# Kernel optimization log

Hardware: AMD Instinct MI355X
Metric: run time of the kernel (lower is better)

Reference implementation:

```python
import jax, jax.numpy as jnp
import numpy as np
from math import sqrt

B, N, CS, H, D, K = 8, 256, 512, 8, 64, 32
NB = 2 * K + 1          # no_bins = 65
CT = 2048               # c_transition
INF = 1e9
WL = sqrt(0.5)          # w_L
EPS = 1e-5


def setup_inputs() -> dict:
    key = jax.random.key(0)
    ks = jax.random.split(key, 10)
    sc = 0.02
    return {
        "s": jax.random.normal(ks[0], (B, N, CS), jnp.float32),
        "masks": jnp.ones((B, N), jnp.bool_),
        "wq": jax.random.normal(ks[1], (CS, D * H), jnp.float32) * sc,
        "wk": jax.random.normal(ks[2], (CS, D * H), jnp.float32) * sc,
        "wv": jax.random.normal(ks[3], (CS, D * H), jnp.float32) * sc,
        "wb": jax.random.normal(ks[4], (NB, H), jnp.float32) * sc,
        "wo": jax.random.normal(ks[5], ((NB + D) * H, CS), jnp.float32) * sc,
        "bo": jnp.zeros((CS,), jnp.float32),
        "ln1_g": jnp.ones((CS,), jnp.float32),
        "ln1_b": jnp.zeros((CS,), jnp.float32),
        "w1": jax.random.normal(ks[6], (CS, CT), jnp.float32) * sc,
        "b1": jnp.zeros((CT,), jnp.float32),
        "w2": jax.random.normal(ks[7], (CT, CS), jnp.float32) * sc,
        "b2": jnp.zeros((CS,), jnp.float32),
        "ln2_g": jnp.ones((CS,), jnp.float32),
        "ln2_b": jnp.zeros((CS,), jnp.float32),
    }


def _layernorm(x, g, b):
    m = jnp.mean(x, -1, keepdims=True)
    v = jnp.var(x, -1, keepdims=True)
    return (x - m) * jax.lax.rsqrt(v + EPS) * g + b


def _heads(x):  # [B,N,D*H] -> [B,H,N,D]  (torch: reshape(B,N,D,H) then move H forward)
    return jnp.transpose(x.reshape(B, N, D, H), (0, 3, 1, 2))


def reference(s, masks, wq, wk, wv, wb, wo, bo, ln1_g, ln1_b, w1, b1, w2, b2, ln2_g, ln2_b):
    mf = masks.astype(s.dtype)                       # [B,N]
    sq = mf[:, :, None] * mf[:, None, :]             # [B,N,N]

    # relative position one-hot, clipped to [-K, K] -> [N,N,NB]
    r = jnp.arange(N)
    dmat = jnp.clip(r[:, None] - r[None, :], -K, K) + K
    relpos_base = jax.nn.one_hot(dmat, NB, dtype=s.dtype)
    relpos = relpos_base[None] * sq[..., None]       # [B,N,N,NB]

    b_bias = jnp.einsum('bijc,ch->bhij', relpos, wb)  # [B,H,N,N]

    q = _heads(s @ wq)                               # [B,H,N,D]
    k = _heads(s @ wk)
    v = _heads(s @ wv)

    logits = WL * (jnp.einsum('bhid,bhjd->bhij', q, k) / sqrt(D) + b_bias)
    logits = logits - INF * (1.0 - sq)[:, None]      # mask
    a = jax.nn.softmax(logits, axis=-1)              # [B,H,N,N]

    # pairwise aggregation and value aggregation (einsum avoids [B,H,N,N,NB] blowup)
    o_pair = jnp.einsum('bhij,bijc->bhic', a, relpos)  # [B,H,N,NB]
    o = jnp.einsum('bhij,bhjd->bhid', a, v)            # [B,H,N,D]

    op = jnp.transpose(o_pair, (0, 2, 1, 3)).reshape(B, N, H * NB)
    ov = jnp.transpose(o, (0, 2, 1, 3)).reshape(B, N, H * D)
    embd = jnp.concatenate([op, ov], axis=-1) @ wo + bo   # [B,N,CS]

    x = _layernorm(s + embd, ln1_g, ln1_b)
    ff = jax.nn.relu(x @ w1 + b1) @ w2 + b2
    x = _layernorm(x + ff, ln2_g, ln2_b)
    return x, a
```

## Files before the change

### kernel.cpp

```cpp
#include <hip/hip_runtime.h>
#include <hip/hip_bf16.h>
#include <cstdint>

#define B_ 8
#define N_ 256
#define CS_ 512
#define H_ 8
#define D_ 64
#define K_ 32
#define NB_ 65
#define CT_ 2048
#define WL_ 0.70710678118654752f

typedef __attribute__((ext_vector_type(8))) short bf16x8;
typedef __attribute__((ext_vector_type(4))) float f32x4;

#define GLOBAL_AS __attribute__((address_space(1)))
#define LDS_AS __attribute__((address_space(3)))

__device__ __forceinline__ void async16(void* lds, const void* g) {
  __builtin_amdgcn_global_load_lds((const GLOBAL_AS uint32_t*)g,
                                   (LDS_AS uint32_t*)lds, 16, 0, 0);
}

__device__ __forceinline__ ushort f2bf(float v) {
  __hip_bfloat16 hb = __float2bfloat16(v);
  return *(ushort*)&hb;
}

__global__ __launch_bounds__(128) void gemm_bf16(
    const ushort* __restrict__ A, const ushort* __restrict__ Bt,
    const float* __restrict__ bias, float* __restrict__ C,
    ushort* __restrict__ Cb, int M, int Nc, int Kd, int flags) {
  __shared__ ushort As[64 * 64];
  __shared__ ushort Bs[128 * 64];
  int tid = threadIdx.x;
  int bm = blockIdx.y * 64, bn = blockIdx.x * 128;
  int S = gridDim.z, z = blockIdx.z;
  int T = Kd >> 6;
  int it0 = (z * T) / S, it1 = ((z + 1) * T) / S;
  if (flags & 8) C += (size_t)z * M * Nc;
  int w = tid >> 6, l = tid & 63;
  int lm = l & 15, lq = l >> 4;
  int srow = tid >> 3;
  int sg = tid & 7;

  f32x4 acc[4][4];
#pragma unroll
  for (int i = 0; i < 4; ++i)
#pragma unroll
    for (int j = 0; j < 4; ++j) acc[i][j] = (f32x4){0.f, 0.f, 0.f, 0.f};

  for (int it = it0; it < it1; ++it) {
    int k0 = it << 6;
    __syncthreads();
#pragma unroll
    for (int r = 0; r < 4; ++r) {
      int row = r * 16 + srow;
      int gl = sg ^ (row & 7);
      async16(&As[row * 64 + sg * 8],
              A + (size_t)(bm + row) * Kd + k0 + gl * 8);
    }
#pragma unroll
    for (int r = 0; r < 8; ++r) {
      int row = r * 16 + srow;
      int gl = sg ^ (row & 7);
      async16(&Bs[row * 64 + sg * 8],
              Bt + (size_t)(bn + row) * Kd + k0 + gl * 8);
    }
    __syncthreads();
#pragma unroll
    for (int kk = 0; kk < 2; ++kk) {
      bf16x8 af[4], bfr[4];
#pragma unroll
      for (int i = 0; i < 4; ++i) {
        int ma = 16 * i + lm;
        af[i] = *(const bf16x8*)&As[ma * 64 + ((kk * 4 + lq) ^ (ma & 7)) * 8];
        int nb = w * 64 + 16 * i + lm;
        bfr[i] = *(const bf16x8*)&Bs[nb * 64 + ((kk * 4 + lq) ^ (nb & 7)) * 8];
      }
#pragma unroll
      for (int i = 0; i < 4; ++i)
#pragma unroll
        for (int j = 0; j < 4; ++j)
          acc[i][j] = __builtin_amdgcn_mfma_f32_16x16x32_bf16(
              af[i], bfr[j], acc[i][j], 0, 0, 0);
    }
  }
#pragma unroll
  for (int j = 0; j < 4; ++j) {
    int col = bn + w * 64 + 16 * j + lm;
    float bv = ((flags & 1) && z == 0) ? bias[col] : 0.f;
#pragma unroll
    for (int i = 0; i < 4; ++i) {
#pragma unroll
      for (int r = 0; r < 4; ++r) {
        int row = bm + 16 * i + lq * 4 + r;
        float v = acc[i][j][r] + bv;
        if (flags & 2) v = fmaxf(v, 0.f);
        if (flags & 8) C[(size_t)row * Nc + col] = v;
        if (flags & 4) Cb[(size_t)row * Nc + col] = f2bf(v);
        if (flags & 16) {
          int which = col >> 9, c = col & 511;
          int hh = c >> 6, d2 = c & 63;
          int bb = row >> 8, nn = row & 255;
          size_t dst;
          if (which == 2)
            dst = (size_t)2 * 1048576 + (((size_t)(bb * 8 + hh) * 64) + d2) * 256 + nn;
          else
            dst = (size_t)which * 1048576 + (((size_t)(bb * 8 + hh) * 256) + nn) * 64 + d2;
          Cb[dst] = f2bf(v);
        }
      }
    }
  }
}

__global__ __launch_bounds__(256) void prep_all(
    const float* __restrict__ s, __hip_bfloat16* __restrict__ s_bf,
    const float* __restrict__ wq, const float* __restrict__ wk,
    const float* __restrict__ wv, const float* __restrict__ wo,
    const float* __restrict__ w1, const float* __restrict__ w2,
    __hip_bfloat16* __restrict__ wqkvT, __hip_bfloat16* __restrict__ wopT,
    __hip_bfloat16* __restrict__ w1T, __hip_bfloat16* __restrict__ w2T) {
  int blk = blockIdx.x;
  if (blk < 1024) {
    int i = blk * 256 + threadIdx.x;
    float4 v = ((const float4*)s)[i];
    s_bf[i * 4 + 0] = __float2bfloat16(v.x);
    s_bf[i * 4 + 1] = __float2bfloat16(v.y);
    s_bf[i * 4 + 2] = __float2bfloat16(v.z);
    s_bf[i * 4 + 3] = __float2bfloat16(v.w);
    return;
  }
  blk -= 1024;
  __shared__ float tile[32][33];
  const float* src;
  __hip_bfloat16* dst;
  int R, C, Kpad, tX, tIdx, whichBase = -1;
  if (blk < 768) {
    int zz = blk >> 8; tIdx = blk & 255;
    src = zz == 0 ? wq : zz == 1 ? wk : wv;
    dst = wqkvT; whichBase = zz * 512; R = 512; C = 512; Kpad = 512; tX = 16;
  } else if (blk < 1312) {
    tIdx = blk - 768; src = wo; dst = wopT; R = 1032; C = 512; Kpad = 1088; tX = 16;
  } else if (blk < 2336) {
    tIdx = blk - 1312; src = w1; dst = w1T; R = 512; C = 2048; Kpad = 512; tX = 64;
  } else {
    tIdx = blk - 2336; src = w2; dst = w2T; R = 2048; C = 512; Kpad = 2048; tX = 16;
  }
  int c0 = (tIdx % tX) * 32, r0 = (tIdx / tX) * 32;
  int tx = threadIdx.x & 31, ty = threadIdx.x >> 5;
#pragma unroll
  for (int yy = 0; yy < 32; yy += 8) {
    int r = r0 + ty + yy, c = c0 + tx;
    tile[ty + yy][tx] = (r < R && c < C) ? src[(size_t)r * C + c] : 0.f;
  }
  __syncthreads();
#pragma unroll
  for (int yy = 0; yy < 32; yy += 8) {
    int cc = c0 + ty + yy, k = r0 + tx;
    if (cc < C && k < Kpad) {
      int n = (whichBase >= 0) ? (whichBase + (cc & 7) * 64 + (cc >> 3)) : cc;
      dst[(size_t)n * Kpad + k] = __float2bfloat16(tile[tx][ty + yy]);
    }
  }
}

__global__ __launch_bounds__(256) void attn_fused(
    const ushort* __restrict__ qh, const ushort* __restrict__ kh,
    const ushort* __restrict__ vT, const int* __restrict__ masks,
    const float* __restrict__ wb, float* __restrict__ a_out,
    ushort* __restrict__ cat) {
  int strip = blockIdx.x & 3, bh = blockIdx.x >> 2;
  int h = bh & 7, b = bh >> 3;
  __shared__ ushort Ks[256 * 64];
  __shared__ ushort Ps[64 * 64];
  __shared__ float wbs[NB_];
  __shared__ float mfj[256];
  int tid = threadIdx.x;
  int srow = tid >> 3, sg = tid & 7;
#pragma unroll
  for (int rr = 0; rr < 8; ++rr) {
    int row = rr * 32 + srow;
    int gl = sg ^ (row & 7);
    async16(&Ks[row * 64 + sg * 8],
            kh + ((size_t)bh * 256 + row) * 64 + gl * 8);
  }
  int w = tid >> 6, l = tid & 63, lm = l & 15, lq = l >> 4;
  bf16x8 qf[2];
  {
    const ushort* qrow =
        qh + ((size_t)bh * 256 + strip * 64 + w * 16 + lm) * 64 + lq * 8;
    qf[0] = *(const bf16x8*)qrow;
    qf[1] = *(const bf16x8*)(qrow + 32);
  }
  if (tid < NB_) wbs[tid] = wb[tid * H_ + h];
  mfj[tid] = (masks[b * 256 + tid] != 0) ? 1.f : 0.f;
  __syncthreads();

  f32x4 acc[16];
#pragma unroll
  for (int ct = 0; ct < 16; ++ct) {
    int krow = ct * 16 + lm;
    bf16x8 kf0 = *(const bf16x8*)&Ks[krow * 64 + ((lq) ^ (krow & 7)) * 8];
    bf16x8 kf1 = *(const bf16x8*)&Ks[krow * 64 + ((4 + lq) ^ (krow & 7)) * 8];
    f32x4 zf = (f32x4){0.f, 0.f, 0.f, 0.f};
    zf = __builtin_amdgcn_mfma_f32_16x16x32_bf16(qf[0], kf0, zf, 0, 0, 0);
    acc[ct] = __builtin_amdgcn_mfma_f32_16x16x32_bf16(qf[1], kf1, zf, 0, 0, 0);
  }
  int ibase = strip * 64 + w * 16 + lq * 4;
  float mfi[4];
#pragma unroll
  for (int r = 0; r < 4; ++r) mfi[r] = mfj[ibase + r];
#pragma unroll
  for (int ct = 0; ct < 16; ++ct) {
    int j = ct * 16 + lm;
    float mj = mfj[j];
#pragma unroll
    for (int r = 0; r < 4; ++r) {
      int i = ibase + r;
      int diff = i - j;
      int cb = diff < -K_ ? 0 : (diff > K_ ? 2 * K_ : diff + K_);
      float sq = mfi[r] * mj;
      acc[ct][r] = WL_ * (acc[ct][r] * 0.125f + wbs[cb] * sq) - 1e9f * (1.f - sq);
    }
  }
  float mx[4], sm[4];
#pragma unroll
  for (int r = 0; r < 4; ++r) {
    float m = acc[0][r];
#pragma unroll
    for (int ct = 1; ct < 16; ++ct) m = fmaxf(m, acc[ct][r]);
#pragma unroll
    for (int o = 1; o < 16; o <<= 1) m = fmaxf(m, __shfl_xor(m, o, 64));
    mx[r] = m;
  }
#pragma unroll
  for (int ct = 0; ct < 16; ++ct)
#pragma unroll
    for (int r = 0; r < 4; ++r) acc[ct][r] = __expf(acc[ct][r] - mx[r]);
#pragma unroll
  for (int r = 0; r < 4; ++r) {
    float s = 0.f;
#pragma unroll
    for (int ct = 0; ct < 16; ++ct) s += acc[ct][r];
#pragma unroll
    for (int o = 1; o < 16; o <<= 1) s += __shfl_xor(s, o, 64);
    sm[r] = 1.f / s;
  }
  float p0[4] = {0.f, 0.f, 0.f, 0.f}, p64[4] = {0.f, 0.f, 0.f, 0.f};
#pragma unroll
  for (int ct = 0; ct < 16; ++ct) {
    int j = ct * 16 + lm;
    float mj = mfj[j];
#pragma unroll
    for (int r = 0; r < 4; ++r) {
      int i = ibase + r;
      float aval = acc[ct][r] * sm[r];
      a_out[((size_t)bh * 256 + i) * 256 + j] = aval;
      float val = aval * mfi[r] * mj;
      int diff = i - j;
      if (diff <= -K_)      p0[r] += val;
      else if (diff >= K_)  p64[r] += val;
      else cat[((size_t)(b * 256 + i)) * 1088 + h * 65 + diff + K_] = f2bf(val);
    }
  }
#pragma unroll
  for (int r = 0; r < 4; ++r)
#pragma unroll
    for (int o = 1; o < 16; o <<= 1) {
      p0[r]  += __shfl_xor(p0[r], o, 64);
      p64[r] += __shfl_xor(p64[r], o, 64);
    }
  if (lm == 0) {
#pragma unroll
    for (int r = 0; r < 4; ++r) {
      int i = ibase + r;
      cat[((size_t)(b * 256 + i)) * 1088 + h * 65 + 0]      = f2bf(p0[r]);
      cat[((size_t)(b * 256 + i)) * 1088 + h * 65 + 2 * K_] = f2bf(p64[r]);
    }
  }
#pragma unroll
  for (int r = 0; r < 4; ++r) {
    int i = ibase + r;
#pragma unroll
    for (int t = 0; t < 4; ++t) {
      int c = 1 + lm + 16 * t;
      if (c < 64) {
        int j = i - c + K_;
        if (j < 0 || j > 255)
          cat[((size_t)(b * 256 + i)) * 1088 + h * 65 + c] = 0;
      }
    }
  }
  if (h == 0) {
    for (int idx = tid; idx < 64 * 56; idx += 256) {
      int r = idx / 56, c = 1032 + (idx - r * 56);
      cat[((size_t)(b * 256 + strip * 64 + r)) * 1088 + c] = 0;
    }
  }
  f32x4 acc2[4];
#pragma unroll
  for (int nt = 0; nt < 4; ++nt) acc2[nt] = (f32x4){0.f, 0.f, 0.f, 0.f};
  const ushort* vbase = vT + (size_t)bh * 16384;
#pragma unroll
  for (int qt = 0; qt < 4; ++qt) {
    bf16x8 vf0[4], vf1[4];
#pragma unroll
    for (int nt = 0; nt < 4; ++nt) {
      const ushort* vrow = vbase + (size_t)(nt * 16 + lm) * 256 + qt * 64 + lq * 8;
      vf0[nt] = *(const bf16x8*)vrow;
      vf1[nt] = *(const bf16x8*)(vrow + 32);
    }
#pragma unroll
    for (int ctl = 0; ctl < 4; ++ctl) {
      int ct = qt * 4 + ctl;
#pragma unroll
      for (int r = 0; r < 4; ++r) {
        int rowl = w * 16 + lq * 4 + r;
        int g = ctl * 2 + (lm >> 3);
        Ps[rowl * 64 + ((g ^ (rowl & 7)) << 3) + (lm & 7)] =
            f2bf(acc[ct][r] * sm[r]);
      }
    }
    int prow = w * 16 + lm;
#pragma unroll
    for (int kst = 0; kst < 2; ++kst) {
      bf16x8 af = *(const bf16x8*)&Ps[prow * 64 + (((kst * 4 + lq) ^ (prow & 7)) << 3)];
#pragma unroll
      for (int nt = 0; nt < 4; ++nt)
        acc2[nt] = __builtin_amdgcn_mfma_f32_16x16x32_bf16(
            af, kst ? vf1[nt] : vf0[nt], acc2[nt], 0, 0, 0);
    }
  }
#pragma unroll
  for (int nt = 0; nt < 4; ++nt) {
    int d = nt * 16 + lm;
#pragma unroll
    for (int r = 0; r < 4; ++r) {
      int i = ibase + r;
      cat[((size_t)(b * 256 + i)) * 1088 + 520 + h * 64 + d] = f2bf(acc2[nt][r]);
    }
  }
}

__device__ __forceinline__ float lnReduceSum(float v, float* red) {
#pragma unroll
  for (int o = 32; o > 0; o >>= 1) v += __shfl_xor(v, o, 64);
  int w = threadIdx.x >> 6;
  __syncthreads();
  if ((threadIdx.x & 63) == 0) red[w] = v;
  __syncthreads();
  return red[0] + red[1] + red[2] + red[3];
}

__global__ __launch_bounds__(256) void ln_sum(
    const float* __restrict__ x1, const float* __restrict__ xp,
    int S, int stride, const float* __restrict__ g,
    const float* __restrict__ bta, float* __restrict__ out,
    __hip_bfloat16* __restrict__ out_bf) {
  __shared__ float red[4];
  int row = blockIdx.x, tid = threadIdx.x;
  size_t base = (size_t)row * 512;
  float v0 = x1[base + tid];
  float v1 = x1[base + tid + 256];
  for (int s = 0; s < S; ++s) {
    v0 += xp[(size_t)s * stride + base + tid];
    v1 += xp[(size_t)s * stride + base + tid + 256];
  }
  float su = lnReduceSum(v0 + v1, red);
  float sq = lnReduceSum(v0 * v0 + v1 * v1, red);
  float mean = su * (1.f / 512.f);
  float var = sq * (1.f / 512.f) - mean * mean;
  float inv = rsqrtf(var + 1e-5f);
  float o0 = (v0 - mean) * inv * g[tid] + bta[tid];
  float o1 = (v1 - mean) * inv * g[tid + 256] + bta[tid + 256];
  out[base + tid]       = o0;
  out[base + tid + 256] = o1;
  if (out_bf) {
    out_bf[base + tid]       = __float2bfloat16(o0);
    out_bf[base + tid + 256] = __float2bfloat16(o1);
  }
}

extern "C" void kernel_launch(void* const* d_in, const int* in_sizes, int n_in,
                              void* d_out, int out_size, void* d_ws, size_t ws_size,
                              hipStream_t stream) {
  const float* s     = (const float*)d_in[0];
  const int*   masks = (const int*)d_in[1];
  const float* wq = (const float*)d_in[2];
  const float* wk = (const float*)d_in[3];
  const float* wv = (const float*)d_in[4];
  const float* wb = (const float*)d_in[5];
  const float* wo = (const float*)d_in[6];
  const float* bo = (const float*)d_in[7];
  const float* ln1_g = (const float*)d_in[8];
  const float* ln1_b = (const float*)d_in[9];
  const float* w1 = (const float*)d_in[10];
  const float* b1 = (const float*)d_in[11];
  const float* w2 = (const float*)d_in[12];
  const float* b2 = (const float*)d_in[13];
  const float* ln2_g = (const float*)d_in[14];
  const float* ln2_b = (const float*)d_in[15];

  float* out_x = (float*)d_out;
  float* out_a = out_x + 1048576;

  float* ws = (float*)d_ws;
  float* embd_part = ws + 0;
  float* xbuf      = ws + 4194304;
  float* ff_part   = ws + 5242880;
  ushort* qkv_bf   = (ushort*)(ws + 9437184);
  ushort* q_bf = qkv_bf;
  ushort* k_bf = qkv_bf + 1048576;
  ushort* v_bf = qkv_bf + 2097152;
  ushort* cat_bf = (ushort*)(ws + 10223616);
  __hip_bfloat16* h_bf  = (__hip_bfloat16*)(ws + 11337728);
  __hip_bfloat16* s_bf  = (__hip_bfloat16*)(ws + 13434880);
  __hip_bfloat16* x_bf  = (__hip_bfloat16*)(ws + 13959168);
  __hip_bfloat16* wqkvT = (__hip_bfloat16*)(ws + 14483456);
  __hip_bfloat16* wopT  = (__hip_bfloat16*)(ws + 14876672);
  __hip_bfloat16* w1T   = (__hip_bfloat16*)(ws + 15155200);
  __hip_bfloat16* w2T   = (__hip_bfloat16*)(ws + 15679488);

  dim3 blk(256), blkg(128);
  prep_all<<<dim3(4384), blk, 0, stream>>>(s, s_bf, wq, wk, wv, wo, w1, w2,
                                           wqkvT, wopT, w1T, w2T);
  gemm_bf16<<<dim3(12, 32, 1), blkg, 0, stream>>>(
      (const ushort*)s_bf, (const ushort*)wqkvT, nullptr, nullptr,
      qkv_bf, 2048, 1536, 512, 16);
  attn_fused<<<dim3(256), blk, 0, stream>>>(q_bf, k_bf, v_bf, masks, wb,
                                            out_a, cat_bf);
  gemm_bf16<<<dim3(4, 32, 4), blkg, 0, stream>>>(
      cat_bf, (const ushort*)wopT, bo, embd_part, nullptr,
      2048, 512, 1088, 1 | 8);
  ln_sum<<<dim3(2048), blk, 0, stream>>>(s, embd_part, 4, 1048576,
                                         ln1_g, ln1_b, xbuf, x_bf);
  gemm_bf16<<<dim3(16, 32, 1), blkg, 0, stream>>>(
      (const ushort*)x_bf, (const ushort*)w1T, b1, nullptr, (ushort*)h_bf,
      2048, 2048, 512, 1 | 2 | 4);
  gemm_bf16<<<dim3(4, 32, 4), blkg, 0, stream>>>(
      (const ushort*)h_bf, (const ushort*)w2T, b2, ff_part, nullptr,
      2048, 512, 2048, 1 | 8);
  ln_sum<<<dim3(2048), blk, 0, stream>>>(xbuf, ff_part, 4, 1048576,
                                         ln2_g, ln2_b, out_x, nullptr);
}
```

Baseline: 194.7 us.

## Stage GEMM bf16 epilogues through LDS, vectorize LN/prep, halve attention block rows

```diff
diff --git a/kernel.cpp b/kernel.cpp
--- a/kernel.cpp
+++ b/kernel.cpp
@@ -87,32 +87,82 @@
               af[i], bfr[j], acc[i][j], 0, 0, 0);
     }
   }
+
+  int bcol0 = bn + w * 64;
+  int lr = l >> 3, lc = l & 7;
+  ushort* Tb = &Bs[w * 4096];
+
+  if (flags & 16) {
+    int which = bcol0 >> 9;
+    int hh = (bcol0 & 511) >> 6;
+    int b = bm >> 8, nn0 = bm & 255;
+    if (which == 2) {
+#pragma unroll
+      for (int j = 0; j < 4; ++j)
+#pragma unroll
+        for (int i = 0; i < 4; ++i) {
+          ushort pk[4];
+#pragma unroll
+          for (int r = 0; r < 4; ++r) pk[r] = f2bf(acc[i][j][r]);
+          *(uint2*)&Tb[(16 * j + lm) * 64 + 16 * i + lq * 4] = *(uint2*)pk;
+        }
+    } else {
+#pragma unroll
+      for (int j = 0; j < 4; ++j)
+#pragma unroll
+        for (int i = 0; i < 4; ++i)
+#pragma unroll
+          for (int r = 0; r < 4; ++r)
+            Tb[(16 * i + lq * 4 + r) * 64 + 16 * j + lm] = f2bf(acc[i][j][r]);
+    }
+    __asm__ __volatile__("" ::: "memory");
+    ushort* dstb = Cb + (size_t)which * 1048576 + (size_t)(b * 8 + hh) * 16384;
+#pragma unroll
+    for (int p = 0; p < 8; ++p) {
+      int rowL = p * 8 + lr;
+      bf16x8 vv = *(const bf16x8*)&Tb[rowL * 64 + lc * 8];
+      if (which == 2)
+        *(bf16x8*)(dstb + (size_t)rowL * 256 + nn0 + lc * 8) = vv;
+      else
+        *(bf16x8*)(dstb + (size_t)(nn0 + rowL) * 64 + lc * 8) = vv;
+    }
+    return;
+  }
+  if (flags & 4) {
+#pragma unroll
+    for (int j = 0; j < 4; ++j) {
+      float bv = ((flags & 1) && z == 0) ? bias[bcol0 + 16 * j + lm] : 0.f;
+#pragma unroll
+      for (int i = 0; i < 4; ++i)
+#pragma unroll
+        for (int r = 0; r < 4; ++r) {
+          float v = acc[i][j][r] + bv;
+          if (flags & 2) v = fmaxf(v, 0.f);
+          Tb[(16 * i + lq * 4 + r) * 64 + 16 * j + lm] = f2bf(v);
+        }
+    }
+    __asm__ __volatile__("" ::: "memory");
+#pragma unroll
+    for (int p = 0; p < 8; ++p) {
+      int rowL = p * 8 + lr;
+      bf16x8 vv = *(const bf16x8*)&Tb[rowL * 64 + lc * 8];
+      *(bf16x8*)(Cb + (size_t)(bm + rowL) * Nc + bcol0 + lc * 8) = vv;
+    }
+    return;
+  }
 #pragma unroll
   for (int j = 0; j < 4; ++j) {
-    int col = bn + w * 64 + 16 * j + lm;
+    int col = bcol0 + 16 * j + lm;
     float bv = ((flags & 1) && z == 0) ? bias[col] : 0.f;
 #pragma unroll
-    for (int i = 0; i < 4; ++i) {
+    for (int i = 0; i < 4; ++i)
 #pragma unroll
       for (int r = 0; r < 4; ++r) {
         int row = bm + 16 * i + lq * 4 + r;
         float v = acc[i][j][r] + bv;
         if (flags & 2) v = fmaxf(v, 0.f);
-        if (flags & 8) C[(size_t)row * Nc + col] = v;
-        if (flags & 4) Cb[(size_t)row * Nc + col] = f2bf(v);
-        if (flags & 16) {
-          int which = col >> 9, c = col & 511;
-          int hh = c >> 6, d2 = c & 63;
-          int bb = row >> 8, nn = row & 255;
-          size_t dst;
-          if (which == 2)
-            dst = (size_t)2 * 1048576 + (((size_t)(bb * 8 + hh) * 64) + d2) * 256 + nn;
-          else
-            dst = (size_t)which * 1048576 + (((size_t)(bb * 8 + hh) * 256) + nn) * 64 + d2;
-          Cb[dst] = f2bf(v);
-        }
+        C[(size_t)row * Nc + col] = v;
       }
-    }
   }
 }
 
@@ -124,16 +174,16 @@
     __hip_bfloat16* __restrict__ wqkvT, __hip_bfloat16* __restrict__ wopT,
     __hip_bfloat16* __restrict__ w1T, __hip_bfloat16* __restrict__ w2T) {
   int blk = blockIdx.x;
-  if (blk < 1024) {
+  if (blk < 512) {
     int i = blk * 256 + threadIdx.x;
-    float4 v = ((const float4*)s)[i];
-    s_bf[i * 4 + 0] = __float2bfloat16(v.x);
-    s_bf[i * 4 + 1] = __float2bfloat16(v.y);
-    s_bf[i * 4 + 2] = __float2bfloat16(v.z);
-    s_bf[i * 4 + 3] = __float2bfloat16(v.w);
+    float4 a = ((const float4*)s)[i * 2];
+    float4 c = ((const float4*)s)[i * 2 + 1];
+    ushort pk[8] = {f2bf(a.x), f2bf(a.y), f2bf(a.z), f2bf(a.w),
+                    f2bf(c.x), f2bf(c.y), f2bf(c.z), f2bf(c.w)};
+    *(uint4*)&((ushort*)s_bf)[i * 8] = *(uint4*)pk;
     return;
   }
-  blk -= 1024;
+  blk -= 512;
   __shared__ float tile[32][33];
   const float* src;
   __hip_bfloat16* dst;
@@ -167,22 +217,22 @@
   }
 }
 
-__global__ __launch_bounds__(256) void attn_fused(
+__global__ __launch_bounds__(128) void attn_fused(
     const ushort* __restrict__ qh, const ushort* __restrict__ kh,
     const ushort* __restrict__ vT, const int* __restrict__ masks,
     const float* __restrict__ wb, float* __restrict__ a_out,
     ushort* __restrict__ cat) {
-  int strip = blockIdx.x & 3, bh = blockIdx.x >> 2;
+  int strip = blockIdx.x & 7, bh = blockIdx.x >> 3;
   int h = bh & 7, b = bh >> 3;
   __shared__ ushort Ks[256 * 64];
-  __shared__ ushort Ps[64 * 64];
+  __shared__ ushort Ps[32 * 64];
   __shared__ float wbs[NB_];
   __shared__ float mfj[256];
   int tid = threadIdx.x;
   int srow = tid >> 3, sg = tid & 7;
 #pragma unroll
-  for (int rr = 0; rr < 8; ++rr) {
-    int row = rr * 32 + srow;
+  for (int rr = 0; rr < 16; ++rr) {
+    int row = rr * 16 + srow;
     int gl = sg ^ (row & 7);
     async16(&Ks[row * 64 + sg * 8],
             kh + ((size_t)bh * 256 + row) * 64 + gl * 8);
@@ -191,12 +241,13 @@
   bf16x8 qf[2];
   {
     const ushort* qrow =
-        qh + ((size_t)bh * 256 + strip * 64 + w * 16 + lm) * 64 + lq * 8;
+        qh + ((size_t)bh * 256 + strip * 32 + w * 16 + lm) * 64 + lq * 8;
     qf[0] = *(const bf16x8*)qrow;
     qf[1] = *(const bf16x8*)(qrow + 32);
   }
   if (tid < NB_) wbs[tid] = wb[tid * H_ + h];
-  mfj[tid] = (masks[b * 256 + tid] != 0) ? 1.f : 0.f;
+  mfj[tid]       = (masks[b * 256 + tid] != 0) ? 1.f : 0.f;
+  mfj[tid + 128] = (masks[b * 256 + tid + 128] != 0) ? 1.f : 0.f;
   __syncthreads();
 
   f32x4 acc[16];
@@ -209,7 +260,7 @@
     zf = __builtin_amdgcn_mfma_f32_16x16x32_bf16(qf[0], kf0, zf, 0, 0, 0);
     acc[ct] = __builtin_amdgcn_mfma_f32_16x16x32_bf16(qf[1], kf1, zf, 0, 0, 0);
   }
-  int ibase = strip * 64 + w * 16 + lq * 4;
+  int ibase = strip * 32 + w * 16 + lq * 4;
   float mfi[4];
 #pragma unroll
   for (int r = 0; r < 4; ++r) mfi[r] = mfj[ibase + r];
@@ -295,9 +346,9 @@
     }
   }
   if (h == 0) {
-    for (int idx = tid; idx < 64 * 56; idx += 256) {
+    for (int idx = tid; idx < 32 * 56; idx += 128) {
       int r = idx / 56, c = 1032 + (idx - r * 56);
-      cat[((size_t)(b * 256 + strip * 64 + r)) * 1088 + c] = 0;
+      cat[((size_t)(b * 256 + strip * 32 + r)) * 1088 + c] = 0;
     }
   }
   f32x4 acc2[4];
@@ -345,42 +396,44 @@
   }
 }
 
-__device__ __forceinline__ float lnReduceSum(float v, float* red) {
-#pragma unroll
-  for (int o = 32; o > 0; o >>= 1) v += __shfl_xor(v, o, 64);
-  int w = threadIdx.x >> 6;
-  __syncthreads();
-  if ((threadIdx.x & 63) == 0) red[w] = v;
-  __syncthreads();
-  return red[0] + red[1] + red[2] + red[3];
-}
-
-__global__ __launch_bounds__(256) void ln_sum(
+__global__ __launch_bounds__(128) void ln_sum(
     const float* __restrict__ x1, const float* __restrict__ xp,
     int S, int stride, const float* __restrict__ g,
     const float* __restrict__ bta, float* __restrict__ out,
     __hip_bfloat16* __restrict__ out_bf) {
-  __shared__ float red[4];
+  __shared__ float redA[2], redB[2];
   int row = blockIdx.x, tid = threadIdx.x;
   size_t base = (size_t)row * 512;
-  float v0 = x1[base + tid];
-  float v1 = x1[base + tid + 256];
+  float4 v = *(const float4*)(x1 + base + tid * 4);
   for (int s = 0; s < S; ++s) {
-    v0 += xp[(size_t)s * stride + base + tid];
-    v1 += xp[(size_t)s * stride + base + tid + 256];
-  }
-  float su = lnReduceSum(v0 + v1, red);
-  float sq = lnReduceSum(v0 * v0 + v1 * v1, red);
+    float4 p = *(const float4*)(xp + (size_t)s * stride + base + tid * 4);
+    v.x += p.x; v.y += p.y; v.z += p.z; v.w += p.w;
+  }
+  float su = v.x + v.y + v.z + v.w;
+  float sq = v.x * v.x + v.y * v.y + v.z * v.z + v.w * v.w;
+#pragma unroll
+  for (int o = 32; o > 0; o >>= 1) {
+    su += __shfl_xor(su, o, 64);
+    sq += __shfl_xor(sq, o, 64);
+  }
+  int w = tid >> 6;
+  if ((tid & 63) == 0) { redA[w] = su; redB[w] = sq; }
+  __syncthreads();
+  su = redA[0] + redA[1]; sq = redB[0] + redB[1];
   float mean = su * (1.f / 512.f);
   float var = sq * (1.f / 512.f) - mean * mean;
   float inv = rsqrtf(var + 1e-5f);
-  float o0 = (v0 - mean) * inv * g[tid] + bta[tid];
-  float o1 = (v1 - mean) * inv * g[tid + 256] + bta[tid + 256];
-  out[base + tid]       = o0;
-  out[base + tid + 256] = o1;
+  float4 gv = *(const float4*)(g + tid * 4);
+  float4 bv = *(const float4*)(bta + tid * 4);
+  float4 o4;
+  o4.x = (v.x - mean) * inv * gv.x + bv.x;
+  o4.y = (v.y - mean) * inv * gv.y + bv.y;
+  o4.z = (v.z - mean) * inv * gv.z + bv.z;
+  o4.w = (v.w - mean) * inv * gv.w + bv.w;
+  *(float4*)(out + base + tid * 4) = o4;
   if (out_bf) {
-    out_bf[base + tid]       = __float2bfloat16(o0);
-    out_bf[base + tid + 256] = __float2bfloat16(o1);
+    ushort pk[4] = {f2bf(o4.x), f2bf(o4.y), f2bf(o4.z), f2bf(o4.w)};
+    *(uint2*)&((ushort*)out_bf)[base + tid * 4] = *(uint2*)pk;
   }
 }
 
@@ -425,24 +478,24 @@
   __hip_bfloat16* w2T   = (__hip_bfloat16*)(ws + 15679488);
 
   dim3 blk(256), blkg(128);
-  prep_all<<<dim3(4384), blk, 0, stream>>>(s, s_bf, wq, wk, wv, wo, w1, w2,
+  prep_all<<<dim3(3872), blk, 0, stream>>>(s, s_bf, wq, wk, wv, wo, w1, w2,
                                            wqkvT, wopT, w1T, w2T);
   gemm_bf16<<<dim3(12, 32, 1), blkg, 0, stream>>>(
       (const ushort*)s_bf, (const ushort*)wqkvT, nullptr, nullptr,
       qkv_bf, 2048, 1536, 512, 16);
-  attn_fused<<<dim3(256), blk, 0, stream>>>(q_bf, k_bf, v_bf, masks, wb,
-                                            out_a, cat_bf);
+  attn_fused<<<dim3(512), blkg, 0, stream>>>(q_bf, k_bf, v_bf, masks, wb,
+                                             out_a, cat_bf);
   gemm_bf16<<<dim3(4, 32, 4), blkg, 0, stream>>>(
       cat_bf, (const ushort*)wopT, bo, embd_part, nullptr,
       2048, 512, 1088, 1 | 8);
-  ln_sum<<<dim3(2048), blk, 0, stream>>>(s, embd_part, 4, 1048576,
-                                         ln1_g, ln1_b, xbuf, x_bf);
+  ln_sum<<<dim3(2048), blkg, 0, stream>>>(s, embd_part, 4, 1048576,
+                                          ln1_g, ln1_b, xbuf, x_bf);
   gemm_bf16<<<dim3(16, 32, 1), blkg, 0, stream>>>(
       (const ushort*)x_bf, (const ushort*)w1T, b1, nullptr, (ushort*)h_bf,
       2048, 2048, 512, 1 | 2 | 4);
   gemm_bf16<<<dim3(4, 32, 4), blkg, 0, stream>>>(
       (const ushort*)h_bf, (const ushort*)w2T, b2, ff_part, nullptr,
       2048, 512, 2048, 1 | 8);
-  ln_sum<<<dim3(2048), blk, 0, stream>>>(xbuf, ff_part, 4, 1048576,
-                                         ln2_g, ln2_b, out_x, nullptr);
-}
+  ln_sum<<<dim3(2048), blkg, 0, stream>>>(xbuf, ff_part, 4, 1048576,
+                                          ln2_g, ln2_b, out_x, nullptr);
+}
```

New measurement: 184.8 us. -5.1%, faster.
